# Kernel tuning notes

Measured on AMD Instinct MI355X. Metric: run time of the kernel, lower is better.

## Reference

```python
import jax, jax.numpy as jnp
import numpy as np

B, D, V, S = 256, 784, 128, 2  # batch, dim, max_val, n_steps
ITER_PER_CYCLE = 10
STEP_SIZES = [0.5] + [0.1] * (ITER_PER_CYCLE - 1)   # sbc: [big_step] + [small_step]*...
BAL_CONSTS = [0.9] + [0.6] * (ITER_PER_CYCLE - 1)   # sbc: [big_bal] + [small_bal]*...
TEMP = 1.0


def setup_inputs() -> dict:
    key = jax.random.key(0)
    k1, k2, k3, k4, k5 = jax.random.split(key, 5)
    x = jax.random.randint(k1, (B, D), 0, V, dtype=jnp.int32)
    W = jax.random.normal(k2, (D, D), dtype=jnp.float32) * (1.0 / D)  # keep energies moderate
    b = jax.random.normal(k3, (D,), dtype=jnp.float32) * 0.1
    # Pre-sampled Gumbel noise for the categorical proposal (one slab per inner step)
    ug = jax.random.uniform(k4, (S, B, D, V), dtype=jnp.float32, minval=1e-6, maxval=1.0 - 1e-6)
    gumbel = -jnp.log(-jnp.log(ug))
    # Uniform draws for the MH accept/reject test
    u = jax.random.uniform(k5, (S, B), dtype=jnp.float32)
    k_iter = 0
    return {"x": x, "W": W, "b": b, "gumbel": gumbel, "u": u, "k_iter": k_iter}


def reference(x, W, b, gumbel, u, k_iter):
    step_size = STEP_SIZES[k_iter % ITER_PER_CYCLE]
    bal = BAL_CONSTS[k_iter % ITER_PER_CYCLE]
    Wsym = 0.5 * (W + W.T)

    def model(xf):                      # energy: [B]
        return 0.5 * jnp.einsum('bi,bi->b', xf, xf @ Wsym) + xf @ b

    def gradf(xf):                      # d(energy)/dx: [B, D]
        return xf @ Wsym + b

    disc = jnp.arange(V, dtype=jnp.float32)[None, None, :]  # [1,1,V]

    def calc_logits(xf, g):
        # term1 - term2 from _calc_logits, fused elementwise over [B, D, V]
        diff = disc - xf[:, :, None]
        return g[:, :, None] * diff * bal - diff * diff * (0.5 / step_size)

    def body(x_cur, inp):
        g_noise, ui = inp
        xf = x_cur.astype(jnp.float32)
        g = gradf(xf)
        logits = calc_logits(xf, g)                                  # [B,D,V]
        x_delta = jnp.argmax(logits + g_noise, axis=-1)              # categorical sample [B,D]
        logp = jax.nn.log_softmax(logits, axis=-1)
        lp_forward = jnp.take_along_axis(logp, x_delta[:, :, None], axis=-1)[..., 0].sum(axis=1)
        xdf = x_delta.astype(jnp.float32)
        gd = gradf(xdf) / TEMP
        logits_d = calc_logits(xdf, gd)
        logp_d = jax.nn.log_softmax(logits_d, axis=-1)
        lp_reverse = jnp.take_along_axis(logp_d, x_cur[:, :, None], axis=-1)[..., 0].sum(axis=1)
        la = model(xdf) - model(xf) + lp_reverse - lp_forward        # log accept ratio [B]
        acc = jnp.exp(la) > ui
        x_new = jnp.where(acc[:, None], x_delta, x_cur).astype(x_cur.dtype)
        return x_new, la

    x_out, las = jax.lax.scan(body, x, (gumbel, u))
    return x_out, las[-1]
```

## Files before the change

kernel.cpp:

```cpp
#include <hip/hip_runtime.h>

#define B_ 256
#define D_ 784
#define V_ 128
#define S_ 2
#define BD (B_ * D_)
#define KSPLIT 8
#define KC 98

__device__ __forceinline__ void get_params(const int* kiter, float& ss, float& bal) {
    int k = kiter[0] % 10;
    ss  = (k == 0) ? 0.5f : 0.1f;
    bal = (k == 0) ? 0.9f : 0.6f;
}

__device__ __forceinline__ double wave_red(double v) {
#pragma unroll
    for (int o = 32; o > 0; o >>= 1) v += __shfl_down(v, o, 64);
    return v;
}

__global__ __launch_bounds__(256) void gemm_splitk(
    const int* __restrict__ Aint, const float* __restrict__ W,
    float* __restrict__ Cp)
{
    const int bt = blockIdx.x, dt = blockIdx.y, kz = blockIdx.z;
    const int tid = threadIdx.x;
    const int k0 = kz * KC, kend = k0 + KC;

    __shared__ float As[64][20];
    __shared__ float Ws[16][68];

    const int tx = tid & 15, ty = tid >> 4;
    const int arow = tid >> 2, ac0 = (tid & 3) * 4;
    const int wrow = tid >> 4, wc0 = (tid & 15) * 4;

    float acc[4][4] = {};

    for (int kb = k0; kb < kend; kb += 16) {
#pragma unroll
        for (int c = 0; c < 4; ++c) {
            int k = kb + ac0 + c;
            As[arow][ac0 + c] = (k < kend) ? (float)Aint[(bt * 64 + arow) * D_ + k] : 0.f;
        }
#pragma unroll
        for (int c = 0; c < 4; ++c) {
            int k = kb + wrow;
            int d = dt * 64 + wc0 + c;
            Ws[wrow][wc0 + c] = (k < kend && d < D_)
                ? 0.5f * (W[k * D_ + d] + W[d * D_ + k]) : 0.f;
        }
        __syncthreads();
#pragma unroll
        for (int kk = 0; kk < 16; kk += 4) {
            float va[4][4], vw[4][4];
#pragma unroll
            for (int i = 0; i < 4; ++i) {
                float4 t = *(const float4*)&As[ty * 4 + i][kk];
                va[i][0] = t.x; va[i][1] = t.y; va[i][2] = t.z; va[i][3] = t.w;
            }
#pragma unroll
            for (int m = 0; m < 4; ++m) {
                float4 t = *(const float4*)&Ws[kk + m][tx * 4];
                vw[m][0] = t.x; vw[m][1] = t.y; vw[m][2] = t.z; vw[m][3] = t.w;
            }
#pragma unroll
            for (int m = 0; m < 4; ++m)
#pragma unroll
                for (int i = 0; i < 4; ++i)
#pragma unroll
                    for (int j = 0; j < 4; ++j)
                        acc[i][j] = fmaf(va[i][m], vw[m][j], acc[i][j]);
        }
        __syncthreads();
    }

#pragma unroll
    for (int i = 0; i < 4; ++i) {
        int bb = bt * 64 + ty * 4 + i;
#pragma unroll
        for (int j = 0; j < 4; ++j) {
            int d = dt * 64 + tx * 4 + j;
            if (d < D_) Cp[(size_t)kz * BD + (size_t)bb * D_ + d] = acc[i][j];
        }
    }
}

__global__ __launch_bounds__(832) void forward_k(
    const int* __restrict__ xin, const float* __restrict__ gpart,
    const float* __restrict__ bvec, const float* __restrict__ gumbel,
    const int* __restrict__ kiter, int s,
    int* __restrict__ x_delta, double* __restrict__ lpf, double* __restrict__ Exf)
{
    const int b = blockIdx.x, tid = threadIdx.x;
    float ss, bal; get_params(kiter, ss, bal);
    const float c2 = 0.5f / ss;

    double lp_acc = 0.0, e_acc = 0.0;

    if (tid < D_) {
        const int d = tid, bd = b * D_ + d;
        const int xi = xin[bd];
        const float xfv = (float)xi;

        float gv = 0.f;
#pragma unroll
        for (int p = 0; p < KSPLIT; ++p) gv += gpart[(size_t)p * BD + bd];
        gv += bvec[d];

        const float a1 = bal * gv;
        const float v0 = xfv + a1 * ss;
        int vm = (int)rintf(v0); vm = min(127, max(0, vm));
        const float dmv = v0 - (float)vm;
        const float Reff = sqrtf(30.0f / c2 + dmv * dmv);
        int lo = max(0, (int)ceilf(v0 - Reff));
        int hi = min(127, (int)floorf(v0 + Reff));
        lo = min(lo, vm); hi = max(hi, vm);

        const float dvm = (float)vm - xfv;
        const float mL = dvm * fmaf(-c2, dvm, a1);

        const float4* __restrict__ gq =
            (const float4*)(gumbel + (((size_t)s * B_ + b) * D_ + d) * V_);
        const int q0 = lo >> 2, qh = hi >> 2;
        float4 quad[4];
#pragma unroll
        for (int j = 0; j < 4; ++j) quad[j] = gq[min(q0 + j, qh)];

        float best = -1e30f; int imax = vm;
        float sum0 = 0.f, sum1 = 0.f;
#pragma unroll
        for (int j = 0; j < 4; ++j) {
            const int qi = q0 + j;
            const bool qok = qi <= qh;
            const float qs[4] = {quad[j].x, quad[j].y, quad[j].z, quad[j].w};
#pragma unroll
            for (int c = 0; c < 4; ++c) {
                int v = 4 * qi + c;
                bool ok = qok && v >= lo && v <= hi;
                float dv = (float)v - xfv;
                float lg = dv * fmaf(-c2, dv, a1);
                float y = ok ? (lg + qs[c]) : -1e30f;
                if (y > best) { best = y; imax = v; }
                float e = expf(lg - mL);
                if (c & 1) sum1 += ok ? e : 0.f; else sum0 += ok ? e : 0.f;
            }
        }
        float lse = mL + logf(sum0 + sum1);
        float dvc = (float)imax - xfv;
        float lch = dvc * fmaf(-c2, dvc, a1);
        lp_acc = (double)(lch - lse);
        e_acc  = (double)xfv * ((double)gv + (double)bvec[d]);
        x_delta[bd] = imax;
    }

    __shared__ double wred[13];
    const int lane = tid & 63, wv = tid >> 6;
    double t = wave_red(lp_acc);
    if (lane == 0) wred[wv] = t;
    __syncthreads();
    if (tid == 0) { double sm = 0; for (int i = 0; i < 13; ++i) sm += wred[i]; lpf[b] = sm; }
    __syncthreads();
    t = wave_red(e_acc);
    if (lane == 0) wred[wv] = t;
    __syncthreads();
    if (tid == 0) { double sm = 0; for (int i = 0; i < 13; ++i) sm += wred[i]; Exf[b] = sm; }
}

__global__ __launch_bounds__(832) void reverse_k(
    const int* __restrict__ xin, int* __restrict__ x_cur,
    const int* __restrict__ x_delta,
    const float* __restrict__ gpart, const float* __restrict__ bvec,
    const float* __restrict__ u, const int* __restrict__ kiter,
    int s, int last, const double* __restrict__ lpf, const double* __restrict__ Exf,
    float* __restrict__ out)
{
    const int b = blockIdx.x, tid = threadIdx.x;
    float ss, bal; get_params(kiter, ss, bal);
    const float c2 = 0.5f / ss;

    double lp_acc = 0.0, e_acc = 0.0;

    if (tid < D_) {
        const int d = tid, bd = b * D_ + d;
        const int xi = xin[bd];
        const int xd = x_delta[bd];
        const float xdv = (float)xd;

        float gv = 0.f;
#pragma unroll
        for (int p = 0; p < KSPLIT; ++p) gv += gpart[(size_t)p * BD + bd];
        gv += bvec[d];

        const float a1 = bal * gv;
        const float v0 = xdv + a1 * ss;
        int vm = (int)rintf(v0); vm = min(127, max(0, vm));
        const float dmv = v0 - (float)vm;
        const float Reff = sqrtf(30.0f / c2 + dmv * dmv);
        int lo = max(0, (int)ceilf(v0 - Reff));
        int hi = min(127, (int)floorf(v0 + Reff));
        lo = min(lo, vm); hi = max(hi, vm);

        const float dvm = (float)vm - xdv;
        const float mL = dvm * fmaf(-c2, dvm, a1);
        float sum0 = 0.f, sum1 = 0.f;
#pragma unroll
        for (int j = 0; j < 16; ++j) {
            int v = lo + j;
            bool ok = v <= hi;
            float dv = (float)v - xdv;
            float lg = dv * fmaf(-c2, dv, a1);
            float e = expf(lg - mL);
            if (j & 1) sum1 += ok ? e : 0.f; else sum0 += ok ? e : 0.f;
        }
        float lse = mL + logf(sum0 + sum1);
        float dvc = (float)xi - xdv;
        float lch = dvc * fmaf(-c2, dvc, a1);
        lp_acc = (double)(lch - lse);
        e_acc  = (double)xdv * ((double)gv + (double)bvec[d]);
    }

    __shared__ double wred[13];
    __shared__ int accept_s;
    __shared__ float la_s;
    const int lane = tid & 63, wv = tid >> 6;

    double t = wave_red(lp_acc);
    if (lane == 0) wred[wv] = t;
    __syncthreads();
    double lpr = 0;
    if (tid == 0) { for (int i = 0; i < 13; ++i) lpr += wred[i]; }
    __syncthreads();
    t = wave_red(e_acc);
    if (lane == 0) wred[wv] = t;
    __syncthreads();
    if (tid == 0) {
        double exd = 0; for (int i = 0; i < 13; ++i) exd += wred[i];
        double la = 0.5 * (exd - Exf[b]) + lpr - lpf[b];
        accept_s = (exp(la) > (double)u[s * B_ + b]) ? 1 : 0;
        la_s = (float)la;
    }
    __syncthreads();

    const int acc = accept_s;
    if (tid < D_) {
        const int bd = b * D_ + tid;
        int xn = acc ? x_delta[bd] : xin[bd];
        x_cur[bd] = xn;
        if (last) out[bd] = (float)xn;
    }
    if (last && tid == 0) out[BD + b] = la_s;
}

extern "C" void kernel_launch(void* const* d_in, const int* in_sizes, int n_in,
                              void* d_out, int out_size, void* d_ws, size_t ws_size,
                              hipStream_t stream)
{
    const int*   x     = (const int*)d_in[0];
    const float* W     = (const float*)d_in[1];
    const float* bv    = (const float*)d_in[2];
    const float* gum   = (const float*)d_in[3];
    const float* u     = (const float*)d_in[4];
    const int*   kiter = (const int*)d_in[5];
    float* out = (float*)d_out;

    char* w = (char*)d_ws;
    size_t off = 0;
    auto carve = [&](size_t bytes) { void* p = w + off; off += (bytes + 511) & ~511ull; return p; };
    int*    x_cur   = (int*)   carve((size_t)BD * 4);
    int*    x_delta = (int*)   carve((size_t)BD * 4);
    float*  gpart   = (float*) carve((size_t)KSPLIT * BD * 4);
    double* lpf     = (double*)carve(B_ * 8);
    double* Exf     = (double*)carve(B_ * 8);
    (void)ws_size; (void)in_sizes; (void)n_in; (void)out_size;

    for (int s = 0; s < S_; ++s) {
        const int* xin = (s == 0) ? x : x_cur;
        gemm_splitk<<<dim3(4, 13, KSPLIT), 256, 0, stream>>>(xin, W, gpart);
        forward_k<<<B_, 832, 0, stream>>>(xin, gpart, bv, gum, kiter, s,
                                          x_delta, lpf, Exf);
        gemm_splitk<<<dim3(4, 13, KSPLIT), 256, 0, stream>>>(x_delta, W, gpart);
        reverse_k<<<B_, 832, 0, stream>>>(xin, x_cur, x_delta, gpart, bv, u, kiter, s,
                                          (s == S_ - 1) ? 1 : 0, lpf, Exf, out);
    }
}
```

Baseline: 383.8 us.

## Fuse symmetric-W matvec into forward/reverse kernels and precompute Wsym once

Precomputes the symmetrized weight matrix and a float copy of x once, then computes the gradient matvec directly inside the forward and reverse sampling kernels (4 batch rows per block) instead of separate split-K GEMM launches with partial buffers. The two energy/log-prob reductions are merged into one reduction per row. This removes the partial-sum write/read traffic and four launches, but runs the GEMM with only 64 blocks and a simple per-thread dot-product loop, risking low occupancy and latency-bound loads.

```diff
diff --git a/kernel.cpp b/kernel.cpp
--- a/kernel.cpp
+++ b/kernel.cpp
@@ -5,8 +5,9 @@
 #define V_ 128
 #define S_ 2
 #define BD (B_ * D_)
-#define KSPLIT 8
-#define KC 98
+#define RPB 4
+#define NBLK (B_ / RPB)
+#define TPB 832
 
 __device__ __forceinline__ void get_params(const int* kiter, float& ss, float& bal) {
     int k = kiter[0] % 10;
@@ -20,236 +21,232 @@
     return v;
 }
 
-__global__ __launch_bounds__(256) void gemm_splitk(
-    const int* __restrict__ Aint, const float* __restrict__ W,
-    float* __restrict__ Cp)
-{
-    const int bt = blockIdx.x, dt = blockIdx.y, kz = blockIdx.z;
+__global__ __launch_bounds__(256) void wsym_xf_k(
+    const float* __restrict__ W, const int* __restrict__ x,
+    float* __restrict__ wsym, float* __restrict__ xf)
+{
+    __shared__ float T[64][65];
     const int tid = threadIdx.x;
-    const int k0 = kz * KC, kend = k0 + KC;
-
-    __shared__ float As[64][20];
-    __shared__ float Ws[16][68];
-
-    const int tx = tid & 15, ty = tid >> 4;
-    const int arow = tid >> 2, ac0 = (tid & 3) * 4;
-    const int wrow = tid >> 4, wc0 = (tid & 15) * 4;
-
-    float acc[4][4] = {};
-
-    for (int kb = k0; kb < kend; kb += 16) {
-#pragma unroll
-        for (int c = 0; c < 4; ++c) {
-            int k = kb + ac0 + c;
-            As[arow][ac0 + c] = (k < kend) ? (float)Aint[(bt * 64 + arow) * D_ + k] : 0.f;
-        }
-#pragma unroll
-        for (int c = 0; c < 4; ++c) {
-            int k = kb + wrow;
-            int d = dt * 64 + wc0 + c;
-            Ws[wrow][wc0 + c] = (k < kend && d < D_)
-                ? 0.5f * (W[k * D_ + d] + W[d * D_ + k]) : 0.f;
-        }
-        __syncthreads();
-#pragma unroll
-        for (int kk = 0; kk < 16; kk += 4) {
-            float va[4][4], vw[4][4];
-#pragma unroll
-            for (int i = 0; i < 4; ++i) {
-                float4 t = *(const float4*)&As[ty * 4 + i][kk];
-                va[i][0] = t.x; va[i][1] = t.y; va[i][2] = t.z; va[i][3] = t.w;
-            }
-#pragma unroll
-            for (int m = 0; m < 4; ++m) {
-                float4 t = *(const float4*)&Ws[kk + m][tx * 4];
-                vw[m][0] = t.x; vw[m][1] = t.y; vw[m][2] = t.z; vw[m][3] = t.w;
-            }
-#pragma unroll
-            for (int m = 0; m < 4; ++m)
-#pragma unroll
-                for (int i = 0; i < 4; ++i)
-#pragma unroll
-                    for (int j = 0; j < 4; ++j)
-                        acc[i][j] = fmaf(va[i][m], vw[m][j], acc[i][j]);
-        }
-        __syncthreads();
-    }
-
-#pragma unroll
-    for (int i = 0; i < 4; ++i) {
-        int bb = bt * 64 + ty * 4 + i;
-#pragma unroll
-        for (int j = 0; j < 4; ++j) {
-            int d = dt * 64 + tx * 4 + j;
-            if (d < D_) Cp[(size_t)kz * BD + (size_t)bb * D_ + d] = acc[i][j];
-        }
-    }
-}
-
-__global__ __launch_bounds__(832) void forward_k(
-    const int* __restrict__ xin, const float* __restrict__ gpart,
-    const float* __restrict__ bvec, const float* __restrict__ gumbel,
-    const int* __restrict__ kiter, int s,
-    int* __restrict__ x_delta, double* __restrict__ lpf, double* __restrict__ Exf)
-{
-    const int b = blockIdx.x, tid = threadIdx.x;
+    const int i0 = blockIdx.x * 64, j0 = blockIdx.y * 64;
+
+#pragma unroll
+    for (int m = 0; m < 16; ++m) {
+        int idx = m * 256 + tid;
+        int r = idx >> 6, c = idx & 63;
+        if (j0 + r < D_ && i0 + c < D_)
+            T[r][c] = W[(j0 + r) * D_ + i0 + c];
+    }
+    __syncthreads();
+#pragma unroll
+    for (int m = 0; m < 16; ++m) {
+        int idx = m * 256 + tid;
+        int r = idx >> 6, c = idx & 63;
+        if (i0 + r < D_ && j0 + c < D_)
+            wsym[(i0 + r) * D_ + j0 + c] =
+                0.5f * (W[(i0 + r) * D_ + j0 + c] + T[c][r]);
+    }
+    const int bid = blockIdx.y * 13 + blockIdx.x;
+    for (int g = bid * 256 + tid; g < BD; g += 169 * 256)
+        xf[g] = (float)x[g];
+}
+
+__global__ __launch_bounds__(TPB) void fwd_fused(
+    const int* __restrict__ xin, const float* __restrict__ xfA,
+    const float* __restrict__ wsym, const float* __restrict__ bvec,
+    const float* __restrict__ gumbel, const int* __restrict__ kiter, int s,
+    int* __restrict__ x_delta, float* __restrict__ xdf,
+    double* __restrict__ qf)
+{
+    const int tid = threadIdx.x, d = tid;
+    const int r0 = blockIdx.x * RPB;
     float ss, bal; get_params(kiter, ss, bal);
     const float c2 = 0.5f / ss;
 
-    double lp_acc = 0.0, e_acc = 0.0;
-
-    if (tid < D_) {
-        const int d = tid, bd = b * D_ + d;
-        const int xi = xin[bd];
-        const float xfv = (float)xi;
-
-        float gv = 0.f;
-#pragma unroll
-        for (int p = 0; p < KSPLIT; ++p) gv += gpart[(size_t)p * BD + bd];
-        gv += bvec[d];
-
-        const float a1 = bal * gv;
-        const float v0 = xfv + a1 * ss;
-        int vm = (int)rintf(v0); vm = min(127, max(0, vm));
-        const float dmv = v0 - (float)vm;
-        const float Reff = sqrtf(30.0f / c2 + dmv * dmv);
-        int lo = max(0, (int)ceilf(v0 - Reff));
-        int hi = min(127, (int)floorf(v0 + Reff));
-        lo = min(lo, vm); hi = max(hi, vm);
-
-        const float dvm = (float)vm - xfv;
-        const float mL = dvm * fmaf(-c2, dvm, a1);
-
-        const float4* __restrict__ gq =
-            (const float4*)(gumbel + (((size_t)s * B_ + b) * D_ + d) * V_);
-        const int q0 = lo >> 2, qh = hi >> 2;
-        float4 quad[4];
-#pragma unroll
-        for (int j = 0; j < 4; ++j) quad[j] = gq[min(q0 + j, qh)];
-
-        float best = -1e30f; int imax = vm;
-        float sum0 = 0.f, sum1 = 0.f;
-#pragma unroll
-        for (int j = 0; j < 4; ++j) {
-            const int qi = q0 + j;
-            const bool qok = qi <= qh;
-            const float qs[4] = {quad[j].x, quad[j].y, quad[j].z, quad[j].w};
-#pragma unroll
-            for (int c = 0; c < 4; ++c) {
-                int v = 4 * qi + c;
-                bool ok = qok && v >= lo && v <= hi;
-                float dv = (float)v - xfv;
-                float lg = dv * fmaf(-c2, dv, a1);
-                float y = ok ? (lg + qs[c]) : -1e30f;
-                if (y > best) { best = y; imax = v; }
-                float e = expf(lg - mL);
-                if (c & 1) sum1 += ok ? e : 0.f; else sum0 += ok ? e : 0.f;
+    double q[RPB] = {};
+
+    if (d < D_) {
+        const int a0 = (r0 + 0) * D_, a1r = (r0 + 1) * D_;
+        const int a2 = (r0 + 2) * D_, a3 = (r0 + 3) * D_;
+        float acc0 = 0.f, acc1 = 0.f, acc2 = 0.f, acc3 = 0.f;
+#pragma unroll 4
+        for (int k = 0; k < D_; ++k) {
+            const float wv = wsym[k * D_ + d];
+            acc0 = fmaf(xfA[a0 + k], wv, acc0);
+            acc1 = fmaf(xfA[a1r + k], wv, acc1);
+            acc2 = fmaf(xfA[a2 + k], wv, acc2);
+            acc3 = fmaf(xfA[a3 + k], wv, acc3);
+        }
+        const float accs[RPB] = {acc0, acc1, acc2, acc3};
+        const float bvd = bvec[d];
+
+#pragma unroll
+        for (int r = 0; r < RPB; ++r) {
+            const int b = r0 + r, bd = b * D_ + d;
+            const int xi = xin[bd];
+            const float xfv = (float)xi;
+            const float gv = accs[r] + bvd;
+
+            const float a1 = bal * gv;
+            const float v0 = xfv + a1 * ss;
+            int vm = (int)rintf(v0); vm = min(127, max(0, vm));
+            const float dmv = v0 - (float)vm;
+            const float Reff = sqrtf(30.0f / c2 + dmv * dmv);
+            int lo = max(0, (int)ceilf(v0 - Reff));
+            int hi = min(127, (int)floorf(v0 + Reff));
+            lo = min(lo, vm); hi = max(hi, vm);
+
+            const float dvm = (float)vm - xfv;
+            const float mL = dvm * fmaf(-c2, dvm, a1);
+
+            const float4* __restrict__ gq =
+                (const float4*)(gumbel + (((size_t)s * B_ + b) * D_ + d) * V_);
+            const int q0 = lo >> 2, qh = hi >> 2;
+            float4 quad[4];
+#pragma unroll
+            for (int j = 0; j < 4; ++j) quad[j] = gq[min(q0 + j, qh)];
+
+            float best = -1e30f; int imax = vm;
+            float sum0 = 0.f, sum1 = 0.f;
+#pragma unroll
+            for (int j = 0; j < 4; ++j) {
+                const int qi = q0 + j;
+                const bool qok = qi <= qh;
+                const float qs[4] = {quad[j].x, quad[j].y, quad[j].z, quad[j].w};
+#pragma unroll
+                for (int c = 0; c < 4; ++c) {
+                    int v = 4 * qi + c;
+                    bool ok = qok && v >= lo && v <= hi;
+                    float dv = (float)v - xfv;
+                    float lg = dv * fmaf(-c2, dv, a1);
+                    float y = ok ? (lg + qs[c]) : -1e30f;
+                    if (y > best) { best = y; imax = v; }
+                    float e = expf(lg - mL);
+                    if (c & 1) sum1 += ok ? e : 0.f; else sum0 += ok ? e : 0.f;
+                }
             }
-        }
-        float lse = mL + logf(sum0 + sum1);
-        float dvc = (float)imax - xfv;
-        float lch = dvc * fmaf(-c2, dvc, a1);
-        lp_acc = (double)(lch - lse);
-        e_acc  = (double)xfv * ((double)gv + (double)bvec[d]);
-        x_delta[bd] = imax;
-    }
-
-    __shared__ double wred[13];
-    const int lane = tid & 63, wv = tid >> 6;
-    double t = wave_red(lp_acc);
-    if (lane == 0) wred[wv] = t;
-    __syncthreads();
-    if (tid == 0) { double sm = 0; for (int i = 0; i < 13; ++i) sm += wred[i]; lpf[b] = sm; }
-    __syncthreads();
-    t = wave_red(e_acc);
-    if (lane == 0) wred[wv] = t;
-    __syncthreads();
-    if (tid == 0) { double sm = 0; for (int i = 0; i < 13; ++i) sm += wred[i]; Exf[b] = sm; }
-}
-
-__global__ __launch_bounds__(832) void reverse_k(
-    const int* __restrict__ xin, int* __restrict__ x_cur,
+            float lse = mL + logf(sum0 + sum1);
+            float dvc = (float)imax - xfv;
+            float lch = dvc * fmaf(-c2, dvc, a1);
+            q[r] = (double)(lch - lse)
+                 + 0.5 * (double)xfv * ((double)gv + (double)bvd);
+            x_delta[bd] = imax;
+            xdf[bd] = (float)imax;
+        }
+    }
+
+    __shared__ double wred[13][RPB];
+    const int lane = tid & 63, wv_ = tid >> 6;
+#pragma unroll
+    for (int r = 0; r < RPB; ++r) {
+        double t = wave_red(q[r]);
+        if (lane == 0) wred[wv_][r] = t;
+    }
+    __syncthreads();
+    if (tid < RPB) {
+        double sm = 0;
+        for (int w = 0; w < 13; ++w) sm += wred[w][tid];
+        qf[r0 + tid] = sm;
+    }
+}
+
+__global__ __launch_bounds__(TPB) void rev_fused(
+    const int* __restrict__ xin, const float* __restrict__ xdfA,
     const int* __restrict__ x_delta,
-    const float* __restrict__ gpart, const float* __restrict__ bvec,
+    const float* __restrict__ wsym, const float* __restrict__ bvec,
     const float* __restrict__ u, const int* __restrict__ kiter,
-    int s, int last, const double* __restrict__ lpf, const double* __restrict__ Exf,
+    int s, int last, const double* __restrict__ qf,
+    int* __restrict__ x_cur, float* __restrict__ xf_out,
     float* __restrict__ out)
 {
-    const int b = blockIdx.x, tid = threadIdx.x;
+    const int tid = threadIdx.x, d = tid;
+    const int r0 = blockIdx.x * RPB;
     float ss, bal; get_params(kiter, ss, bal);
     const float c2 = 0.5f / ss;
 
-    double lp_acc = 0.0, e_acc = 0.0;
-
-    if (tid < D_) {
-        const int d = tid, bd = b * D_ + d;
-        const int xi = xin[bd];
-        const int xd = x_delta[bd];
-        const float xdv = (float)xd;
-
-        float gv = 0.f;
-#pragma unroll
-        for (int p = 0; p < KSPLIT; ++p) gv += gpart[(size_t)p * BD + bd];
-        gv += bvec[d];
-
-        const float a1 = bal * gv;
-        const float v0 = xdv + a1 * ss;
-        int vm = (int)rintf(v0); vm = min(127, max(0, vm));
-        const float dmv = v0 - (float)vm;
-        const float Reff = sqrtf(30.0f / c2 + dmv * dmv);
-        int lo = max(0, (int)ceilf(v0 - Reff));
-        int hi = min(127, (int)floorf(v0 + Reff));
-        lo = min(lo, vm); hi = max(hi, vm);
-
-        const float dvm = (float)vm - xdv;
-        const float mL = dvm * fmaf(-c2, dvm, a1);
-        float sum0 = 0.f, sum1 = 0.f;
-#pragma unroll
-        for (int j = 0; j < 16; ++j) {
-            int v = lo + j;
-            bool ok = v <= hi;
-            float dv = (float)v - xdv;
-            float lg = dv * fmaf(-c2, dv, a1);
-            float e = expf(lg - mL);
-            if (j & 1) sum1 += ok ? e : 0.f; else sum0 += ok ? e : 0.f;
-        }
-        float lse = mL + logf(sum0 + sum1);
-        float dvc = (float)xi - xdv;
-        float lch = dvc * fmaf(-c2, dvc, a1);
-        lp_acc = (double)(lch - lse);
-        e_acc  = (double)xdv * ((double)gv + (double)bvec[d]);
-    }
-
-    __shared__ double wred[13];
-    __shared__ int accept_s;
-    __shared__ float la_s;
-    const int lane = tid & 63, wv = tid >> 6;
-
-    double t = wave_red(lp_acc);
-    if (lane == 0) wred[wv] = t;
-    __syncthreads();
-    double lpr = 0;
-    if (tid == 0) { for (int i = 0; i < 13; ++i) lpr += wred[i]; }
-    __syncthreads();
-    t = wave_red(e_acc);
-    if (lane == 0) wred[wv] = t;
-    __syncthreads();
-    if (tid == 0) {
-        double exd = 0; for (int i = 0; i < 13; ++i) exd += wred[i];
-        double la = 0.5 * (exd - Exf[b]) + lpr - lpf[b];
-        accept_s = (exp(la) > (double)u[s * B_ + b]) ? 1 : 0;
-        la_s = (float)la;
-    }
-    __syncthreads();
-
-    const int acc = accept_s;
-    if (tid < D_) {
-        const int bd = b * D_ + tid;
-        int xn = acc ? x_delta[bd] : xin[bd];
-        x_cur[bd] = xn;
-        if (last) out[bd] = (float)xn;
-    }
-    if (last && tid == 0) out[BD + b] = la_s;
+    double q[RPB] = {};
+
+    if (d < D_) {
+        const int a0 = (r0 + 0) * D_, a1r = (r0 + 1) * D_;
+        const int a2 = (r0 + 2) * D_, a3 = (r0 + 3) * D_;
+        float acc0 = 0.f, acc1 = 0.f, acc2 = 0.f, acc3 = 0.f;
+#pragma unroll 4
+        for (int k = 0; k < D_; ++k) {
+            const float wv = wsym[k * D_ + d];
+            acc0 = fmaf(xdfA[a0 + k], wv, acc0);
+            acc1 = fmaf(xdfA[a1r + k], wv, acc1);
+            acc2 = fmaf(xdfA[a2 + k], wv, acc2);
+            acc3 = fmaf(xdfA[a3 + k], wv, acc3);
+        }
+        const float accs[RPB] = {acc0, acc1, acc2, acc3};
+        const float bvd = bvec[d];
+
+#pragma unroll
+        for (int r = 0; r < RPB; ++r) {
+            const int b = r0 + r, bd = b * D_ + d;
+            const int xi = xin[bd];
+            const int xd = x_delta[bd];
+            const float xdv = (float)xd;
+            const float gv = accs[r] + bvd;
+
+            const float a1 = bal * gv;
+            const float v0 = xdv + a1 * ss;
+            int vm = (int)rintf(v0); vm = min(127, max(0, vm));
+            const float dmv = v0 - (float)vm;
+            const float Reff = sqrtf(30.0f / c2 + dmv * dmv);
+            int lo = max(0, (int)ceilf(v0 - Reff));
+            int hi = min(127, (int)floorf(v0 + Reff));
+            lo = min(lo, vm); hi = max(hi, vm);
+
+            const float dvm = (float)vm - xdv;
+            const float mL = dvm * fmaf(-c2, dvm, a1);
+            float sum0 = 0.f, sum1 = 0.f;
+#pragma unroll
+            for (int j = 0; j < 16; ++j) {
+                int v = lo + j;
+                bool ok = v <= hi;
+                float dv = (float)v - xdv;
+                float lg = dv * fmaf(-c2, dv, a1);
+                float e = expf(lg - mL);
+                if (j & 1) sum1 += ok ? e : 0.f; else sum0 += ok ? e : 0.f;
+            }
+            float lse = mL + logf(sum0 + sum1);
+            float dvc = (float)xi - xdv;
+            float lch = dvc * fmaf(-c2, dvc, a1);
+            q[r] = (double)(lch - lse)
+                 + 0.5 * (double)xdv * ((double)gv + (double)bvd);
+        }
+    }
+
+    __shared__ double wred[13][RPB];
+    __shared__ int acc_s[RPB];
+    __shared__ float la_s[RPB];
+    const int lane = tid & 63, wv_ = tid >> 6;
+#pragma unroll
+    for (int r = 0; r < RPB; ++r) {
+        double t = wave_red(q[r]);
+        if (lane == 0) wred[wv_][r] = t;
+    }
+    __syncthreads();
+    if (tid < RPB) {
+        double sm = 0;
+        for (int w = 0; w < 13; ++w) sm += wred[w][tid];
+        double la = sm - qf[r0 + tid];
+        acc_s[tid] = (exp(la) > (double)u[s * B_ + r0 + tid]) ? 1 : 0;
+        la_s[tid] = (float)la;
+    }
+    __syncthreads();
+
+    if (d < D_) {
+#pragma unroll
+        for (int r = 0; r < RPB; ++r) {
+            const int bd = (r0 + r) * D_ + d;
+            int xn = acc_s[r] ? x_delta[bd] : xin[bd];
+            x_cur[bd] = xn;
+            xf_out[bd] = (float)xn;
+            if (last) out[bd] = (float)xn;
+        }
+    }
+    if (last && tid < RPB) out[BD + r0 + tid] = la_s[tid];
 }
 
 extern "C" void kernel_launch(void* const* d_in, const int* in_sizes, int n_in,
@@ -267,20 +264,22 @@
     char* w = (char*)d_ws;
     size_t off = 0;
     auto carve = [&](size_t bytes) { void* p = w + off; off += (bytes + 511) & ~511ull; return p; };
+    float*  wsym    = (float*) carve((size_t)D_ * D_ * 4);
     int*    x_cur   = (int*)   carve((size_t)BD * 4);
     int*    x_delta = (int*)   carve((size_t)BD * 4);
-    float*  gpart   = (float*) carve((size_t)KSPLIT * BD * 4);
-    double* lpf     = (double*)carve(B_ * 8);
-    double* Exf     = (double*)carve(B_ * 8);
+    float*  xf      = (float*) carve((size_t)BD * 4);
+    float*  xdf     = (float*) carve((size_t)BD * 4);
+    double* qf      = (double*)carve(B_ * 8);
     (void)ws_size; (void)in_sizes; (void)n_in; (void)out_size;
+
+    wsym_xf_k<<<dim3(13, 13), 256, 0, stream>>>(W, x, wsym, xf);
 
     for (int s = 0; s < S_; ++s) {
         const int* xin = (s == 0) ? x : x_cur;
-        gemm_splitk<<<dim3(4, 13, KSPLIT), 256, 0, stream>>>(xin, W, gpart);
-        forward_k<<<B_, 832, 0, stream>>>(xin, gpart, bv, gum, kiter, s,
-                                          x_delta, lpf, Exf);
-        gemm_splitk<<<dim3(4, 13, KSPLIT), 256, 0, stream>>>(x_delta, W, gpart);
-        reverse_k<<<B_, 832, 0, stream>>>(xin, x_cur, x_delta, gpart, bv, u, kiter, s,
-                                          (s == S_ - 1) ? 1 : 0, lpf, Exf, out);
-    }
-}
+        fwd_fused<<<NBLK, TPB, 0, stream>>>(xin, xf, wsym, bv, gum, kiter, s,
+                                            x_delta, xdf, qf);
+        rev_fused<<<NBLK, TPB, 0, stream>>>(xin, xdf, x_delta, wsym, bv, u, kiter,
+                                            s, (s == S_ - 1) ? 1 : 0, qf,
+                                            x_cur, xf, out);
+    }
+}
```

Measured after the change: 633.2 us. 65.0% more time.
